# Kernel optimization log

Measured on AMD Instinct MI355X. Metric: run time of the kernel, lower is better.

Reference implementation:

```python
import jax, jax.numpy as jnp
import numpy as np

NUM_GRAPHS = 1024
NODES_PER_GRAPH = 116
DEG = 32
IN_CH = 116
HID = 32
EPS = 1e-5


def setup_inputs() -> dict:
    key = jax.random.key(0)
    ks = jax.random.split(key, 16)
    N = NUM_GRAPHS * NODES_PER_GRAPH
    E = N * DEG
    x = jax.random.normal(ks[0], (N, IN_CH), dtype=jnp.float32)
    # edges stay within each graph: graph id per edge, then random src/dst node in that graph
    gid = jnp.arange(E, dtype=jnp.int64) // (NODES_PER_GRAPH * DEG)
    off = gid * NODES_PER_GRAPH
    src = off + jax.random.randint(ks[1], (E,), 0, NODES_PER_GRAPH, dtype=jnp.int64)
    dst = off + jax.random.randint(ks[2], (E,), 0, NODES_PER_GRAPH, dtype=jnp.int64)
    edge_index = jnp.stack([src, dst], axis=0)
    edge_weight = jax.random.uniform(ks[3], (E,), dtype=jnp.float32)
    batch = jnp.arange(N, dtype=jnp.int64) // NODES_PER_GRAPH
    xavier = lambda k, fi, fo: jax.random.uniform(k, (fi, fo), jnp.float32, -1.0, 1.0) * np.sqrt(6.0 / (fi + fo))
    return {
        "x": x, "edge_index": edge_index, "edge_weight": edge_weight, "batch": batch,
        "W1": xavier(ks[4], IN_CH, HID), "b1": jnp.zeros((HID,), jnp.float32),
        "g1": jnp.ones((HID,), jnp.float32), "be1": jnp.zeros((HID,), jnp.float32),
        "W2": xavier(ks[5], HID, 2 * HID), "b2": jnp.zeros((2 * HID,), jnp.float32),
        "g2": jnp.ones((2 * HID,), jnp.float32), "be2": jnp.zeros((2 * HID,), jnp.float32),
        "Wf1": xavier(ks[6], 4 * HID, HID), "bf1": jnp.zeros((HID,), jnp.float32),
        "gf": jnp.ones((HID,), jnp.float32), "bef": jnp.zeros((HID,), jnp.float32),
        "Wf2": xavier(ks[7], HID, 2), "bf2": jnp.zeros((2,), jnp.float32),
    }


def _gcn_conv(x, row, col, ew, W, b):
    """PyG GCNConv: linear -> add self-loops -> sym-normalized scatter-add -> +bias."""
    N = x.shape[0]
    h = x @ W  # [N, out]
    loop = jnp.arange(N, dtype=row.dtype)
    row_sl = jnp.concatenate([row, loop])
    col_sl = jnp.concatenate([col, loop])
    w_sl = jnp.concatenate([ew, jnp.ones((N,), ew.dtype)])
    deg = jax.ops.segment_sum(w_sl, col_sl, num_segments=N)
    dinv = jnp.where(deg > 0, jax.lax.rsqrt(deg), 0.0)
    norm = dinv[row_sl] * w_sl * dinv[col_sl]  # [E+N]
    msg = h[row_sl] * norm[:, None]            # gather + scale
    out = jax.ops.segment_sum(msg, col_sl, num_segments=N)
    return out + b


def _bn(x, g, b):
    # BatchNorm1d in training mode: biased batch stats over axis 0
    m = jnp.mean(x, axis=0)
    v = jnp.mean(jnp.square(x - m), axis=0)
    return (x - m) * jax.lax.rsqrt(v + EPS) * g + b


def reference(x, edge_index, edge_weight, batch, W1, b1, g1, be1, W2, b2, g2, be2,
              Wf1, bf1, gf, bef, Wf2, bf2):
    row, col = edge_index[0], edge_index[1]
    h = jax.nn.relu(_bn(_gcn_conv(x, row, col, edge_weight, W1, b1), g1, be1))
    h = jax.nn.relu(_bn(_gcn_conv(h, row, col, edge_weight, W2, b2), g2, be2))
    # global mean / max pool over graphs
    counts = jax.ops.segment_sum(jnp.ones((h.shape[0],), h.dtype), batch, num_segments=NUM_GRAPHS)
    x_mean = jax.ops.segment_sum(h, batch, num_segments=NUM_GRAPHS) / counts[:, None]
    x_max = jax.ops.segment_max(h, batch, num_segments=NUM_GRAPHS)
    emb = jnp.concatenate([x_mean, x_max], axis=1)  # [G, 4*HID]
    z = jax.nn.relu(_bn(emb @ Wf1 + bf1, gf, bef))  # dropout = identity (eval)
    return z @ Wf2 + bf2  # [G, num_classes]
```

## Files before the change

### kernel.cpp

```cpp
#include <hip/hip_runtime.h>

#define NPG 116
#define EPG (NPG * 32)
#define HID 32
#define HID2 64
#define EPS 1e-5f

#define WFS 132
#define AS 136
#define YSS 40
#define WBI 58
#define WBTOT (NPG * WBI)
#define HPG (NPG * HID2)

using bf16x8 = __attribute__((ext_vector_type(8))) short;
using f32x4  = __attribute__((ext_vector_type(4))) float;

__device__ __forceinline__ unsigned short f2bf(float f) {
  union { float f; unsigned int i; } cv;
  cv.f = f;
  unsigned int x = cv.i;
  x += 0x7fff + ((x >> 16) & 1);
  return (unsigned short)(x >> 16);
}

#define MFMA16(a, b, c) __builtin_amdgcn_mfma_f32_16x16x32_bf16((a), (b), (c), 0, 0, 0)


__global__ __launch_bounds__(1024) void k_conv1(const float* __restrict__ x,
                                                const int* __restrict__ ei,
                                                const float* __restrict__ ew,
                                                const float* __restrict__ W1,
                                                float* __restrict__ h1,
                                                float* __restrict__ dinvg,
                                                float* __restrict__ stats,
                                                float* __restrict__ buf,
                                                int N, int E) {
  __shared__ __align__(16) float Wf[NPG * WFS];
  __shared__ __align__(16) short W1T[HID * AS];
  __shared__ __align__(16) short L1T[HID * AS];
  __shared__ float degs[NPG];
  __shared__ float ss[HID], qs[HID];
  const int g = blockIdx.x, tid = threadIdx.x;
  const int nb = g * NPG, e0 = g * EPG;
  const int* rowp = ei;
  const int* colp = ei + E;
  const int l = tid & 63, w = tid >> 6;
  const int rf = l & 15, kg = l >> 4;

  for (int i = tid; i < NPG; i += 1024) degs[i] = 1.0f;
  if (tid < HID) { ss[tid] = 0.0f; qs[tid] = 0.0f; }
  { float4* p = (float4*)Wf;
    for (int i = tid; i < NPG * WFS / 4; i += 1024) p[i] = make_float4(0,0,0,0); }
  { int* p = (int*)L1T;
    for (int i = tid; i < HID * AS / 2; i += 1024) p[i] = 0; }
  { int* p = (int*)W1T;
    for (int i = tid; i < HID * AS / 2; i += 1024) p[i] = 0; }
  __syncthreads();
  for (int i = tid; i < NPG * HID; i += 1024) {
    int k = i >> 5, c = i & 31;
    W1T[c * AS + k] = (short)f2bf(W1[i]);
  }
  __syncthreads();

  for (int e = tid; e < EPG; e += 1024) {
    int eg = e0 + e;
    int s = rowp[eg] - nb, d = colp[eg] - nb;
    float wv = ew[eg];
    atomicAdd(&degs[d], wv);
    atomicAdd(&Wf[d * WFS + s], wv);
  }
  if (tid < NPG) atomicAdd(&Wf[tid * WFS + tid], 1.0f);

  const int mt = w >> 1, nt = w & 1;
  const int rl = mt * 16 + rf;
  f32x4 acc1 = {0.f, 0.f, 0.f, 0.f};
#pragma unroll
  for (int kk = 0; kk < 4; ++kk) {
    bf16x8 a;
    if (rl < NPG) {
      const float* xr = x + (size_t)(nb + rl) * NPG;
      if (kk < 3) {
        const float4* xp = (const float4*)(xr + kk * 32 + kg * 8);
        float4 v0 = xp[0], v1 = xp[1];
        a[0] = (short)f2bf(v0.x); a[1] = (short)f2bf(v0.y);
        a[2] = (short)f2bf(v0.z); a[3] = (short)f2bf(v0.w);
        a[4] = (short)f2bf(v1.x); a[5] = (short)f2bf(v1.y);
        a[6] = (short)f2bf(v1.z); a[7] = (short)f2bf(v1.w);
      } else {
        const int k0 = 96 + kg * 8;
#pragma unroll
        for (int j = 0; j < 8; ++j) {
          int k = k0 + j;
          a[j] = (k < NPG) ? (short)f2bf(xr[k]) : (short)0;
        }
      }
    } else {
#pragma unroll
      for (int j = 0; j < 8; ++j) a[j] = 0;
    }
    bf16x8 b = *(const bf16x8*)&W1T[(nt * 16 + rf) * AS + kk * 32 + kg * 8];
    acc1 = MFMA16(a, b, acc1);
  }
  __syncthreads();

#pragma unroll
  for (int i = 0; i < 4; ++i) {
    int row = mt * 16 + kg * 4 + i;
    if (row < NPG)
      L1T[(nt * 16 + rf) * AS + row] = (short)f2bf(rsqrtf(degs[row]) * acc1[i]);
  }
  if (tid < NPG) dinvg[nb + tid] = rsqrtf(degs[tid]);
  {
    int* wbg = (int*)(buf + (size_t)g * HPG);
    for (int idx = tid; idx < WBTOT; idx += 1024) {
      int r = idx / WBI, jj = idx - r * WBI;
      float2 v = *(const float2*)&Wf[r * WFS + 2 * jj];
      wbg[idx] = (unsigned)f2bf(v.x) | ((unsigned)f2bf(v.y) << 16);
    }
  }
  __syncthreads();

  {
    f32x4 acc = {0.f, 0.f, 0.f, 0.f};
#pragma unroll
    for (int kk = 0; kk < 4; ++kk) {
      bf16x8 a;
      if (rl < NPG) {
        const float4* wp = (const float4*)&Wf[rl * WFS + kk * 32 + kg * 8];
        float4 v0 = wp[0], v1 = wp[1];
        a[0] = (short)f2bf(v0.x); a[1] = (short)f2bf(v0.y);
        a[2] = (short)f2bf(v0.z); a[3] = (short)f2bf(v0.w);
        a[4] = (short)f2bf(v1.x); a[5] = (short)f2bf(v1.y);
        a[6] = (short)f2bf(v1.z); a[7] = (short)f2bf(v1.w);
      } else {
#pragma unroll
        for (int j = 0; j < 8; ++j) a[j] = 0;
      }
      bf16x8 b = *(const bf16x8*)&L1T[(nt * 16 + rf) * AS + kk * 32 + kg * 8];
      acc = MFMA16(a, b, acc);
    }
    const int col = nt * 16 + rf;
    float s_ = 0.f, q_ = 0.f;
#pragma unroll
    for (int i = 0; i < 4; ++i) {
      int row = mt * 16 + kg * 4 + i;
      if (row < NPG) {
        float v = rsqrtf(degs[row]) * acc[i];
        h1[(size_t)(nb + row) * HID + col] = v;
        s_ += v; q_ += v * v;
      }
    }
    atomicAdd(&ss[col], s_);
    atomicAdd(&qs[col], q_);
  }
  __syncthreads();
  if (tid < HID) {
    atomicAdd(&stats[tid], ss[tid]);
    atomicAdd(&stats[32 + tid], qs[tid]);
  }
}

__global__ __launch_bounds__(1024) void k_conv2(const float* __restrict__ h1,
                                                const float* __restrict__ W2,
                                                const float* __restrict__ g1,
                                                const float* __restrict__ be1,
                                                const float* __restrict__ stats,
                                                const float* __restrict__ dinvg,
                                                float* __restrict__ buf,
                                                float* __restrict__ stats2,
                                                float invN, int N) {
  __shared__ __align__(16) short Ab[128 * AS];
  __shared__ __align__(16) short ysb[128 * YSS];
  __shared__ __align__(16) short W2T[HID2 * YSS];
  __shared__ __align__(16) short L2T[HID2 * AS];
  __shared__ float dv[NPG];
  __shared__ float ss[HID2], qs[HID2];
  __shared__ float a1s[HID], c1s[HID];
  const int g = blockIdx.x, tid = threadIdx.x;
  const int nb = g * NPG;
  const int l = tid & 63, w = tid >> 6;
  const int rf = l & 15, kg = l >> 4;
  float* bufg = buf + (size_t)g * HPG;

  if (tid < HID) {
    float m = stats[tid] * invN;
    float v = stats[32 + tid] * invN - m * m;
    float a = g1[tid] * rsqrtf(v + EPS);
    a1s[tid] = a;
    c1s[tid] = be1[tid] - m * a;
  }
  if (tid < HID2) { ss[tid] = 0.0f; qs[tid] = 0.0f; }
  { int* p = (int*)Ab;
    for (int i = tid; i < 128 * AS / 2; i += 1024) p[i] = 0; }
  { int* p = (int*)L2T;
    for (int i = tid; i < HID2 * AS / 2; i += 1024) p[i] = 0; }
  for (int i = tid; i < HID * HID2; i += 1024) {
    int k = i >> 6, c = i & 63;
    W2T[c * YSS + k] = (short)f2bf(W2[i]);
  }
  for (int i = tid; i < NPG; i += 1024) dv[i] = dinvg[nb + i];
  __syncthreads();

  {
    const float4* hg = (const float4*)(h1 + (size_t)nb * HID);
    for (int i = tid; i < NPG * 8; i += 1024) {
      int r = i >> 3, kc = i & 7, k0 = kc * 4;
      float4 hv = hg[i];
      float dr = dv[r];
      float y0 = dr * fmaxf(0.f, a1s[k0 + 0] * hv.x + c1s[k0 + 0]);
      float y1 = dr * fmaxf(0.f, a1s[k0 + 1] * hv.y + c1s[k0 + 1]);
      float y2 = dr * fmaxf(0.f, a1s[k0 + 2] * hv.z + c1s[k0 + 2]);
      float y3 = dr * fmaxf(0.f, a1s[k0 + 3] * hv.w + c1s[k0 + 3]);
      unsigned int* yp = (unsigned int*)&ysb[r * YSS + k0];
      yp[0] = (unsigned)f2bf(y0) | ((unsigned)f2bf(y1) << 16);
      yp[1] = (unsigned)f2bf(y2) | ((unsigned)f2bf(y3) << 16);
    }
    const int* wbg = (const int*)bufg;
    int* ab = (int*)Ab;
    for (int idx = tid; idx < WBTOT; idx += 1024) {
      int r = idx / WBI, jj = idx - r * WBI;
      ab[r * (AS / 2) + jj] = wbg[idx];
    }
  }
  __syncthreads();

#pragma unroll
  for (int half = 0; half < 2; ++half) {
    const int t = w + 16 * half;
    const int mt = t >> 2, nt = t & 3;
    bf16x8 a = *(const bf16x8*)&ysb[(mt * 16 + rf) * YSS + kg * 8];
    bf16x8 b = *(const bf16x8*)&W2T[(nt * 16 + rf) * YSS + kg * 8];
    f32x4 acc = {0.f, 0.f, 0.f, 0.f};
    acc = MFMA16(a, b, acc);
    const int col = nt * 16 + rf;
#pragma unroll
    for (int i = 0; i < 4; ++i) {
      int row = mt * 16 + kg * 4 + i;
      if (row < NPG) L2T[col * AS + row] = (short)f2bf(acc[i]);
    }
  }
  __syncthreads();

  {
    const int mt = w >> 1, ntp = (w & 1) * 2;
    f32x4 acc[2] = {{0.f,0.f,0.f,0.f},{0.f,0.f,0.f,0.f}};
#pragma unroll
    for (int kk = 0; kk < 4; ++kk) {
      bf16x8 a = *(const bf16x8*)&Ab[(mt * 16 + rf) * AS + kk * 32 + kg * 8];
#pragma unroll
      for (int u = 0; u < 2; ++u) {
        bf16x8 b = *(const bf16x8*)&L2T[((ntp + u) * 16 + rf) * AS + kk * 32 + kg * 8];
        acc[u] = MFMA16(a, b, acc[u]);
      }
    }
#pragma unroll
    for (int u = 0; u < 2; ++u) {
      const int col = (ntp + u) * 16 + rf;
      float s_ = 0.f, q_ = 0.f;
#pragma unroll
      for (int i = 0; i < 4; ++i) {
        int row = mt * 16 + kg * 4 + i;
        if (row < NPG) {
          float v = dv[row] * acc[u][i];
          bufg[row * HID2 + col] = v;
          s_ += v; q_ += v * v;
        }
      }
      atomicAdd(&ss[col], s_);
      atomicAdd(&qs[col], q_);
    }
  }
  __syncthreads();
  if (tid < HID2) {
    atomicAdd(&stats2[tid], ss[tid]);
    atomicAdd(&stats2[64 + tid], qs[tid]);
  }
}

__global__ __launch_bounds__(256) void k_pool(const float* __restrict__ buf,
                                              const float* __restrict__ g2,
                                              const float* __restrict__ be2,
                                              const float* __restrict__ stats2,
                                              const float* __restrict__ Wf1,
                                              float* __restrict__ z,
                                              float invN, int N) {
  __shared__ float4 psum4[256], pmax4[256];
  __shared__ __align__(16) float emb[128];
  __shared__ __align__(16) float a2s[HID2], c2s[HID2];
  int g = blockIdx.x, tid = threadIdx.x;
  if (tid < HID2) {
    float m = stats2[tid] * invN;
    float v = stats2[64 + tid] * invN - m * m;
    float a = g2[tid] * rsqrtf(v + EPS);
    a2s[tid] = a;
    c2s[tid] = be2[tid] - m * a;
  }
  __syncthreads();
  int c4 = tid & 15, rg = tid >> 4;
  float4 av = ((const float4*)a2s)[c4], bv = ((const float4*)c2s)[c4];
  const float4* h4 = (const float4*)(buf + (size_t)g * HPG);
  float4 s = {0.f, 0.f, 0.f, 0.f};
  float4 mx = {-1e30f, -1e30f, -1e30f, -1e30f};
  for (int n = rg; n < NPG; n += 16) {
    float4 v = h4[n * 16 + c4];
    float4 y;
    y.x = fmaxf(0.f, av.x * v.x + bv.x);
    y.y = fmaxf(0.f, av.y * v.y + bv.y);
    y.z = fmaxf(0.f, av.z * v.z + bv.z);
    y.w = fmaxf(0.f, av.w * v.w + bv.w);
    s.x += y.x; s.y += y.y; s.z += y.z; s.w += y.w;
    mx.x = fmaxf(mx.x, y.x); mx.y = fmaxf(mx.y, y.y);
    mx.z = fmaxf(mx.z, y.z); mx.w = fmaxf(mx.w, y.w);
  }
  psum4[rg * 16 + c4] = s;
  pmax4[rg * 16 + c4] = mx;
  __syncthreads();
  if (tid < 16) {
    float4 S = psum4[tid], M = pmax4[tid];
    for (int j = 1; j < 16; ++j) {
      float4 p = psum4[j * 16 + tid], q = pmax4[j * 16 + tid];
      S.x += p.x; S.y += p.y; S.z += p.z; S.w += p.w;
      M.x = fmaxf(M.x, q.x); M.y = fmaxf(M.y, q.y);
      M.z = fmaxf(M.z, q.z); M.w = fmaxf(M.w, q.w);
    }
    const float inv = 1.0f / NPG;
    ((float4*)emb)[tid] = make_float4(S.x * inv, S.y * inv, S.z * inv, S.w * inv);
    ((float4*)emb)[16 + tid] = M;
  }
  __syncthreads();
  if (tid < 32) {
    float acc = 0.0f;
#pragma unroll
    for (int k = 0; k < 128; ++k) acc += emb[k] * Wf1[k * 32 + tid];
    z[g * 32 + tid] = acc;
  }
}

__global__ __launch_bounds__(256) void k_final(const float* __restrict__ z,
                                               const float* __restrict__ gf,
                                               const float* __restrict__ bef,
                                               const float* __restrict__ Wf2,
                                               const float* __restrict__ bf2,
                                               float* __restrict__ out, int G) {
  __shared__ float ss[32], qs[32], af[32], cf[32];
  __shared__ float w2s[64], b2s[2];
  int tid = threadIdx.x;
  if (tid < 32) { ss[tid] = 0.0f; qs[tid] = 0.0f; }
  if (tid < 64) w2s[tid] = Wf2[tid];
  if (tid < 2) b2s[tid] = bf2[tid];
  __syncthreads();
  const float4* z4 = (const float4*)z;
  int n4 = G * 8;
  float4 s = {0.f, 0.f, 0.f, 0.f}, q = {0.f, 0.f, 0.f, 0.f};
  for (int i = tid; i < n4; i += 256) {
    float4 v = z4[i];
    s.x += v.x; s.y += v.y; s.z += v.z; s.w += v.w;
    q.x += v.x * v.x; q.y += v.y * v.y; q.z += v.z * v.z; q.w += v.w * v.w;
  }
  int cg = (tid & 7) * 4;
  atomicAdd(&ss[cg + 0], s.x); atomicAdd(&ss[cg + 1], s.y);
  atomicAdd(&ss[cg + 2], s.z); atomicAdd(&ss[cg + 3], s.w);
  atomicAdd(&qs[cg + 0], q.x); atomicAdd(&qs[cg + 1], q.y);
  atomicAdd(&qs[cg + 2], q.z); atomicAdd(&qs[cg + 3], q.w);
  __syncthreads();
  if (tid < 32) {
    float invG = 1.0f / G;
    float m = ss[tid] * invG;
    float v = qs[tid] * invG - m * m;
    float a = gf[tid] * rsqrtf(v + EPS);
    af[tid] = a;
    cf[tid] = bef[tid] - m * a;
  }
  __syncthreads();
  for (int g = tid; g < G; g += 256) {
    float o0 = b2s[0], o1 = b2s[1];
    const float4* zr = z4 + g * 8;
#pragma unroll
    for (int kc = 0; kc < 8; ++kc) {
      float4 v = zr[kc];
      int j = 4 * kc;
      float y;
      y = fmaxf(0.f, af[j + 0] * v.x + cf[j + 0]);
      o0 += y * w2s[2 * (j + 0)]; o1 += y * w2s[2 * (j + 0) + 1];
      y = fmaxf(0.f, af[j + 1] * v.y + cf[j + 1]);
      o0 += y * w2s[2 * (j + 1)]; o1 += y * w2s[2 * (j + 1) + 1];
      y = fmaxf(0.f, af[j + 2] * v.z + cf[j + 2]);
      o0 += y * w2s[2 * (j + 2)]; o1 += y * w2s[2 * (j + 2) + 1];
      y = fmaxf(0.f, af[j + 3] * v.w + cf[j + 3]);
      o0 += y * w2s[2 * (j + 3)]; o1 += y * w2s[2 * (j + 3) + 1];
    }
    out[g * 2] = o0;
    out[g * 2 + 1] = o1;
  }
}

extern "C" void kernel_launch(void* const* d_in, const int* in_sizes, int n_in,
                              void* d_out, int out_size, void* d_ws, size_t ws_size,
                              hipStream_t stream) {
  const float* x   = (const float*)d_in[0];
  const int*   ei  = (const int*)d_in[1];
  const float* ew  = (const float*)d_in[2];
  const float* W1  = (const float*)d_in[4];
  const float* g1  = (const float*)d_in[6];
  const float* be1 = (const float*)d_in[7];
  const float* W2  = (const float*)d_in[8];
  const float* g2  = (const float*)d_in[10];
  const float* be2 = (const float*)d_in[11];
  const float* Wf1 = (const float*)d_in[12];
  const float* gf  = (const float*)d_in[14];
  const float* bef = (const float*)d_in[15];
  const float* Wf2 = (const float*)d_in[16];
  const float* bf2 = (const float*)d_in[17];

  int N = in_sizes[3];
  int E = in_sizes[2];
  int G = N / NPG;

  float* ws    = (float*)d_ws;
  float* stats = ws;
  float* dinv  = ws + 256;
  float* h1    = dinv + N;
  float* buf   = h1 + (size_t)N * HID;
  float* z     = buf + (size_t)G * HPG;
  float* out   = (float*)d_out;
  float invN   = 1.0f / (float)N;

  hipMemsetAsync(stats, 0, 256 * sizeof(float), stream);
  k_conv1<<<G, 1024, 0, stream>>>(x, ei, ew, W1, h1, dinv, stats, buf, N, E);
  k_conv2<<<G, 1024, 0, stream>>>(h1, W2, g1, be1, stats, dinv, buf,
                                  stats + 64, invN, N);
  k_pool<<<G, 256, 0, stream>>>(buf, g2, be2, stats + 64, Wf1, z, invN, N);
  k_final<<<1, 256, 0, stream>>>(z, gf, bef, Wf2, bf2, out, G);
}
```

Baseline: 153.5 us.

## Split first linear transform into separate kernel and pad adjacency rows

Moves the x@W1 MFMA projection out of k_conv1 into a new 256-thread kernel k_lin1 that writes bf16 results into the h1 workspace region. k_conv1 then reads those values back and scales them by dinv, instead of loading x itself. The adjacency buffer rows are also padded to 64 ints, so index math uses shifts instead of division by 58. The aim is to shrink k_conv1's shared memory and latency, at the cost of an extra launch and an extra global round-trip for the projected features.

```diff
diff --git a/kernel.cpp b/kernel.cpp
--- a/kernel.cpp
+++ b/kernel.cpp
@@ -9,9 +9,7 @@
 #define WFS 132
 #define AS 136
 #define YSS 40
-#define WBI 58
-#define WBTOT (NPG * WBI)
-#define HPG (NPG * HID2)
+#define HPG 7424
 
 using bf16x8 = __attribute__((ext_vector_type(8))) short;
 using f32x4  = __attribute__((ext_vector_type(4))) float;
@@ -23,21 +21,83 @@
   x += 0x7fff + ((x >> 16) & 1);
   return (unsigned short)(x >> 16);
 }
+__device__ __forceinline__ float bf2f(unsigned int u) {
+  union { unsigned int i; float f; } cv;
+  cv.i = u << 16;
+  return cv.f;
+}
 
 #define MFMA16(a, b, c) __builtin_amdgcn_mfma_f32_16x16x32_bf16((a), (b), (c), 0, 0, 0)
 
 
-__global__ __launch_bounds__(1024) void k_conv1(const float* __restrict__ x,
-                                                const int* __restrict__ ei,
+__global__ __launch_bounds__(256) void k_lin1(const float* __restrict__ x,
+                                              const float* __restrict__ W1,
+                                              float* __restrict__ h1reg,
+                                              int N) {
+  __shared__ __align__(16) short W1T[HID * AS];
+  const int g = blockIdx.x, tid = threadIdx.x;
+  const int nb = g * NPG;
+  const int l = tid & 63, w = tid >> 6;
+  const int rf = l & 15, kg = l >> 4;
+
+  { int* p = (int*)W1T;
+    for (int i = tid; i < HID * AS / 2; i += 256) p[i] = 0; }
+  __syncthreads();
+  for (int i = tid; i < NPG * HID; i += 256) {
+    int k = i >> 5, c = i & 31;
+    W1T[c * AS + k] = (short)f2bf(W1[i]);
+  }
+  __syncthreads();
+
+  unsigned short* lb = (unsigned short*)(h1reg + (size_t)g * 3712);
+  for (int t = w; t < 16; t += 4) {
+    const int mt = t >> 1, nt = t & 1;
+    const int rl = mt * 16 + rf;
+    f32x4 acc = {0.f, 0.f, 0.f, 0.f};
+#pragma unroll
+    for (int kk = 0; kk < 4; ++kk) {
+      bf16x8 a;
+      if (rl < NPG) {
+        const float* xr = x + (size_t)(nb + rl) * NPG;
+        if (kk < 3) {
+          const float4* xp = (const float4*)(xr + kk * 32 + kg * 8);
+          float4 v0 = xp[0], v1 = xp[1];
+          a[0] = (short)f2bf(v0.x); a[1] = (short)f2bf(v0.y);
+          a[2] = (short)f2bf(v0.z); a[3] = (short)f2bf(v0.w);
+          a[4] = (short)f2bf(v1.x); a[5] = (short)f2bf(v1.y);
+          a[6] = (short)f2bf(v1.z); a[7] = (short)f2bf(v1.w);
+        } else {
+          const int k0 = 96 + kg * 8;
+#pragma unroll
+          for (int j = 0; j < 8; ++j) {
+            int k = k0 + j;
+            a[j] = (k < NPG) ? (short)f2bf(xr[k]) : (short)0;
+          }
+        }
+      } else {
+#pragma unroll
+        for (int j = 0; j < 8; ++j) a[j] = 0;
+      }
+      bf16x8 b = *(const bf16x8*)&W1T[(nt * 16 + rf) * AS + kk * 32 + kg * 8];
+      acc = MFMA16(a, b, acc);
+    }
+    const int col = nt * 16 + rf;
+#pragma unroll
+    for (int i = 0; i < 4; ++i) {
+      int row = mt * 16 + kg * 4 + i;
+      if (row < NPG) lb[row * HID + col] = f2bf(acc[i]);
+    }
+  }
+}
+
+__global__ __launch_bounds__(1024) void k_conv1(const int* __restrict__ ei,
                                                 const float* __restrict__ ew,
-                                                const float* __restrict__ W1,
-                                                float* __restrict__ h1,
+                                                float* __restrict__ h1reg,
                                                 float* __restrict__ dinvg,
                                                 float* __restrict__ stats,
                                                 float* __restrict__ buf,
                                                 int N, int E) {
   __shared__ __align__(16) float Wf[NPG * WFS];
-  __shared__ __align__(16) short W1T[HID * AS];
   __shared__ __align__(16) short L1T[HID * AS];
   __shared__ float degs[NPG];
   __shared__ float ss[HID], qs[HID];
@@ -54,13 +114,6 @@
     for (int i = tid; i < NPG * WFS / 4; i += 1024) p[i] = make_float4(0,0,0,0); }
   { int* p = (int*)L1T;
     for (int i = tid; i < HID * AS / 2; i += 1024) p[i] = 0; }
-  { int* p = (int*)W1T;
-    for (int i = tid; i < HID * AS / 2; i += 1024) p[i] = 0; }
-  __syncthreads();
-  for (int i = tid; i < NPG * HID; i += 1024) {
-    int k = i >> 5, c = i & 31;
-    W1T[c * AS + k] = (short)f2bf(W1[i]);
-  }
   __syncthreads();
 
   for (int e = tid; e < EPG; e += 1024) {
@@ -71,57 +124,35 @@
     atomicAdd(&Wf[d * WFS + s], wv);
   }
   if (tid < NPG) atomicAdd(&Wf[tid * WFS + tid], 1.0f);
-
-  const int mt = w >> 1, nt = w & 1;
-  const int rl = mt * 16 + rf;
-  f32x4 acc1 = {0.f, 0.f, 0.f, 0.f};
-#pragma unroll
-  for (int kk = 0; kk < 4; ++kk) {
-    bf16x8 a;
-    if (rl < NPG) {
-      const float* xr = x + (size_t)(nb + rl) * NPG;
-      if (kk < 3) {
-        const float4* xp = (const float4*)(xr + kk * 32 + kg * 8);
-        float4 v0 = xp[0], v1 = xp[1];
-        a[0] = (short)f2bf(v0.x); a[1] = (short)f2bf(v0.y);
-        a[2] = (short)f2bf(v0.z); a[3] = (short)f2bf(v0.w);
-        a[4] = (short)f2bf(v1.x); a[5] = (short)f2bf(v1.y);
-        a[6] = (short)f2bf(v1.z); a[7] = (short)f2bf(v1.w);
-      } else {
-        const int k0 = 96 + kg * 8;
-#pragma unroll
-        for (int j = 0; j < 8; ++j) {
-          int k = k0 + j;
-          a[j] = (k < NPG) ? (short)f2bf(xr[k]) : (short)0;
-        }
-      }
-    } else {
-#pragma unroll
-      for (int j = 0; j < 8; ++j) a[j] = 0;
-    }
-    bf16x8 b = *(const bf16x8*)&W1T[(nt * 16 + rf) * AS + kk * 32 + kg * 8];
-    acc1 = MFMA16(a, b, acc1);
-  }
-  __syncthreads();
-
-#pragma unroll
-  for (int i = 0; i < 4; ++i) {
-    int row = mt * 16 + kg * 4 + i;
-    if (row < NPG)
-      L1T[(nt * 16 + rf) * AS + row] = (short)f2bf(rsqrtf(degs[row]) * acc1[i]);
-  }
+  __syncthreads();
+
   if (tid < NPG) dinvg[nb + tid] = rsqrtf(degs[tid]);
   {
+    const unsigned int* lb32 =
+        (const unsigned int*)(h1reg + (size_t)g * 3712);
+    for (int i = tid; i < NPG * 16; i += 1024) {
+      int row = i >> 4, c2 = (i & 15) * 2;
+      unsigned int u = lb32[i];
+      float dr = rsqrtf(degs[row]);
+      L1T[c2 * AS + row] = (short)f2bf(bf2f(u & 0xffffu) * dr);
+      L1T[(c2 + 1) * AS + row] = (short)f2bf(bf2f(u >> 16) * dr);
+    }
     int* wbg = (int*)(buf + (size_t)g * HPG);
-    for (int idx = tid; idx < WBTOT; idx += 1024) {
-      int r = idx / WBI, jj = idx - r * WBI;
-      float2 v = *(const float2*)&Wf[r * WFS + 2 * jj];
-      wbg[idx] = (unsigned)f2bf(v.x) | ((unsigned)f2bf(v.y) << 16);
+    for (int idx = tid; idx < NPG * 64; idx += 1024) {
+      int r = idx >> 6, jj = idx & 63;
+      int val = 0;
+      if (jj < 58) {
+        float2 v = *(const float2*)&Wf[r * WFS + 2 * jj];
+        val = (unsigned)f2bf(v.x) | ((unsigned)f2bf(v.y) << 16);
+      }
+      wbg[idx] = val;
     }
   }
   __syncthreads();
 
   {
+    const int mt = w >> 1, nt = w & 1;
+    const int rl = mt * 16 + rf;
     f32x4 acc = {0.f, 0.f, 0.f, 0.f};
 #pragma unroll
     for (int kk = 0; kk < 4; ++kk) {
@@ -147,7 +178,7 @@
       int row = mt * 16 + kg * 4 + i;
       if (row < NPG) {
         float v = rsqrtf(degs[row]) * acc[i];
-        h1[(size_t)(nb + row) * HID + col] = v;
+        h1reg[(size_t)(nb + row) * HID + col] = v;
         s_ += v; q_ += v * v;
       }
     }
@@ -218,8 +249,8 @@
     }
     const int* wbg = (const int*)bufg;
     int* ab = (int*)Ab;
-    for (int idx = tid; idx < WBTOT; idx += 1024) {
-      int r = idx / WBI, jj = idx - r * WBI;
+    for (int idx = tid; idx < NPG * 64; idx += 1024) {
+      int r = idx >> 6, jj = idx & 63;
       ab[r * (AS / 2) + jj] = wbg[idx];
     }
   }
@@ -427,7 +458,8 @@
   float invN   = 1.0f / (float)N;
 
   hipMemsetAsync(stats, 0, 256 * sizeof(float), stream);
-  k_conv1<<<G, 1024, 0, stream>>>(x, ei, ew, W1, h1, dinv, stats, buf, N, E);
+  k_lin1<<<G, 256, 0, stream>>>(x, W1, h1, N);
+  k_conv1<<<G, 1024, 0, stream>>>(ei, ew, h1, dinv, stats, buf, N, E);
   k_conv2<<<G, 1024, 0, stream>>>(h1, W2, g1, be1, stats, dinv, buf,
                                   stats + 64, invN, N);
   k_pool<<<G, 256, 0, stream>>>(buf, g2, be2, stats + 64, Wf1, z, invN, N);
```

Result: slower. 168.9 us (+10.0%).
